# Performance work log

Measured on AMD Instinct MI355X. Metric: run time of the kernel, lower is better.

Reference implementation:

```python
import jax, jax.numpy as jnp
import numpy as np

IN_DIM, OUT_DIM, NUM, K = 256, 128, 16, 3
BATCH = 2048
MONO = ((0, 1), (1, -1))  # (input dim index, direction)


def _make_grid():
    # linspace over grid_range, then extend k knots on each side with uniform step h
    lo, hi = -1.0, 1.0
    h = (hi - lo) / NUM
    pts = np.linspace(lo, hi, NUM + 1)
    ext = np.concatenate([lo + h * np.arange(-K, 0), pts, hi + h * np.arange(1, K + 1)])
    return jnp.asarray(np.tile(ext, (IN_DIM, 1)), dtype=jnp.float32)  # (in_dim, num+2k+1)


def _b_batch(x, grid, k):
    # de-Boor B-spline basis. x: (B, in), grid: (in, G). Returns (B, in, G-k-1).
    xg = x[:, :, None]
    g = grid[None, :, :]
    B = ((xg >= g[:, :, :-1]) & (xg < g[:, :, 1:])).astype(x.dtype)
    for p in range(1, k + 1):
        left = (xg - g[:, :, :-(p + 1)]) / (g[:, :, p:-1] - g[:, :, :-(p + 1)]) * B[:, :, :-1]
        right = (g[:, :, p + 1:] - xg) / (g[:, :, p + 1:] - g[:, :, 1:-p]) * B[:, :, 1:]
        B = left + right
    return B


def setup_inputs() -> dict:
    key = jax.random.key(0)
    k1, k2, k3, k4 = jax.random.split(key, 4)
    inv_sqrt_in = 1.0 / np.sqrt(IN_DIM)
    x = 0.4 * jax.random.normal(k1, (BATCH, IN_DIM), dtype=jnp.float32)
    coef = 0.1 * jax.random.normal(k2, (IN_DIM, OUT_DIM, NUM + K), dtype=jnp.float32)
    scale_sp_raw = jnp.ones((IN_DIM, OUT_DIM), dtype=jnp.float32) * inv_sqrt_in
    scale_base = (jax.random.uniform(k3, (IN_DIM, OUT_DIM), dtype=jnp.float32) * 2.0 - 1.0) * inv_sqrt_in
    grid = _make_grid()
    mask = jnp.ones((IN_DIM, OUT_DIM), dtype=jnp.float32)
    base_mask = jnp.ones((IN_DIM, OUT_DIM), dtype=jnp.float32)
    for dim, _ in MONO:
        base_mask = base_mask.at[dim, :].set(0.0)
    return {"x": x, "coef": coef, "scale_sp_raw": scale_sp_raw, "scale_base": scale_base,
            "grid": grid, "mask": mask, "base_mask": base_mask}


def reference(x, coef, scale_sp_raw, scale_base, grid, mask, base_mask):
    bs = x.shape[0]
    preacts = jnp.broadcast_to(x[:, None, :], (bs, OUT_DIM, IN_DIM))
    # monotonic reparameterization: softplus + cumsum over spline-coefficient axis
    for dim, direction in MONO:
        delta = jnp.cumsum(jax.nn.softplus(coef[dim]), axis=-1)  # (out, num+k)
        coef = coef.at[dim].set(direction * delta)
    # coef2curve: basis (B, in, num+k) contracted with coef (in, out, num+k)
    basis = _b_batch(x, grid, K)
    y = jnp.einsum('bid,iod->bio', basis, coef)  # (B, in, out)
    postspline = jnp.transpose(y, (0, 2, 1))
    scale_sp = jax.nn.softplus(scale_sp_raw)
    y = scale_sp[None, :, :] * y
    base = base_mask * scale_base[None, :, :] * jax.nn.silu(x)[:, :, None]
    y = y + base
    y = mask[None, :, :] * y
    postacts = jnp.transpose(y, (0, 2, 1))
    out = jnp.sum(y, axis=1)  # (B, out)
    return out, preacts, postacts, postspline
```

## Files before the change

### kernel.cpp

```cpp
#include <hip/hip_runtime.h>
#include <math.h>

#define IN_DIM   256
#define OUT_DIM  128
#define NCOEF    19
#define BATCH    2048
#define BT       4

__device__ __forceinline__ float softplus_f(float v) {
  return (v > 20.0f) ? v : log1pf(expf(v));
}

__global__ void kan_prep(const float* __restrict__ coef,
                         const float* __restrict__ ssp,
                         const float* __restrict__ sbase,
                         const float* __restrict__ mask,
                         const float* __restrict__ bmask,
                         float* __restrict__ coefT,
                         float* __restrict__ At,
                         float* __restrict__ Bt) {
  int g = blockIdx.x * 256 + threadIdx.x;
  int o = g >> 8;
  int i = g & 255;
  const float* src = coef + ((size_t)i * OUT_DIM + o) * NCOEF;
  float c[NCOEF];
#pragma unroll
  for (int d = 0; d < NCOEF; ++d) c[d] = src[d];
  if (i < 2) {
    float dir = (i == 0) ? 1.0f : -1.0f;
    float acc = 0.0f;
#pragma unroll
    for (int d = 0; d < NCOEF; ++d) { acc += softplus_f(c[d]); c[d] = dir * acc; }
  }
  float* dst = coefT + (size_t)g * NCOEF;
#pragma unroll
  for (int d = 0; d < NCOEF; ++d) dst[d] = c[d];
  int io = i * OUT_DIM + o;
  float m = mask[io];
  At[g] = m * softplus_f(ssp[io]);
  Bt[g] = m * bmask[io] * sbase[io];
}

__device__ __forceinline__ float wave_reduce(float v) {
  int t;
  t = __builtin_amdgcn_update_dpp(0, __float_as_int(v), 0x111, 0xf, 0xf, true); v += __int_as_float(t);
  t = __builtin_amdgcn_update_dpp(0, __float_as_int(v), 0x112, 0xf, 0xf, true); v += __int_as_float(t);
  t = __builtin_amdgcn_update_dpp(0, __float_as_int(v), 0x114, 0xf, 0xf, true); v += __int_as_float(t);
  t = __builtin_amdgcn_update_dpp(0, __float_as_int(v), 0x118, 0xf, 0xf, true); v += __int_as_float(t);
  t = __builtin_amdgcn_update_dpp(0, __float_as_int(v), 0x142, 0xa, 0xf, true); v += __int_as_float(t);
  t = __builtin_amdgcn_update_dpp(0, __float_as_int(v), 0x143, 0xc, 0xf, true); v += __int_as_float(t);
  return v;
}

__global__ __launch_bounds__(512) void kan_main(
    const float* __restrict__ x,
    const float* __restrict__ coefT,
    const float* __restrict__ At,
    const float* __restrict__ Bt,
    float* __restrict__ out,
    float* __restrict__ preacts,
    float* __restrict__ postacts,
    float* __restrict__ postspline) {
  __shared__ __align__(16) float s_coef[IN_DIM * NCOEF];
  __shared__ float s_out[BT][OUT_DIM][4];

  const int tid  = threadIdx.x;
  const int i    = tid & 255;
  const int bsub = tid >> 8;
  const int wq   = (tid >> 6) & 3;
  const int b0   = blockIdx.x * BT;

  float xv[2], sl[2], wv[2][4];
  int   wi[2][4];

#pragma unroll
  for (int bb = 0; bb < 2; ++bb) {
    int b = b0 + bsub * 2 + bb;
    float xx = x[(size_t)b * IN_DIM + i];
    xv[bb] = xx;
    sl[bb] = xx / (1.0f + expf(-xx));

    float tpos = (xx + 1.375f) * 8.0f;
    int j = (int)floorf(tpos);
    bool valid = (j >= 0) && (j <= 21);
    int jc = valid ? j : 3;

    float N[4] = {1.0f, 0.0f, 0.0f, 0.0f};
#pragma unroll
    for (int p = 1; p <= 3; ++p) {
      const float inv = (p == 1) ? 8.0f : ((p == 2) ? 4.0f : (8.0f / 3.0f));
      float Np[4] = {0.0f, 0.0f, 0.0f, 0.0f};
#pragma unroll
      for (int m = 0; m < 4; ++m) {
        if (m <= p) {
          float ga = -1.375f + 0.125f * (float)(jc + m - p);
          float v = 0.0f;
          if (m > 0) v += (xx - ga) * inv * N[m - 1];
          if (m < p) v += ((ga + 0.125f * (float)(p + 1)) - xx) * inv * N[m];
          Np[m] = v;
        }
      }
#pragma unroll
      for (int m = 0; m < 4; ++m) N[m] = Np[m];
    }
#pragma unroll
    for (int r = 0; r < 4; ++r) {
      int dr = jc - 3 + r;
      bool ok = valid && (dr >= 0) && (dr <= 18);
      wv[bb][r] = ok ? N[r] : 0.0f;
      wi[bb][r] = i * NCOEF + (ok ? dr : 0);
    }
  }

  for (int o = 0; o < OUT_DIM; ++o) {
    __syncthreads();
    {
      const float4* src4 = (const float4*)(coefT + (size_t)o * (IN_DIM * NCOEF));
      float4* dst4 = (float4*)s_coef;
      for (int t = tid; t < (IN_DIM * NCOEF) / 4; t += 512) dst4[t] = src4[t];
    }
    __syncthreads();

    float a_sc = At[o * IN_DIM + i];
    float b_sc = Bt[o * IN_DIM + i];

#pragma unroll
    for (int bb = 0; bb < 2; ++bb) {
      int bl = bsub * 2 + bb;
      float sp = wv[bb][0] * s_coef[wi[bb][0]]
               + wv[bb][1] * s_coef[wi[bb][1]]
               + wv[bb][2] * s_coef[wi[bb][2]]
               + wv[bb][3] * s_coef[wi[bb][3]];
      float ya = a_sc * sp + b_sc * sl[bb];

      size_t off = (((size_t)(b0 + bl) * OUT_DIM) + o) * IN_DIM + i;
      __builtin_nontemporal_store(sp,     postspline + off);
      __builtin_nontemporal_store(ya,     postacts   + off);
      __builtin_nontemporal_store(xv[bb], preacts    + off);

      float red = wave_reduce(ya);
      if ((tid & 63) == 63) s_out[bl][o][wq] = red;
    }
  }

  __syncthreads();
  {
    int bl = tid >> 7;
    int o  = tid & 127;
    float s = s_out[bl][o][0] + s_out[bl][o][1] + s_out[bl][o][2] + s_out[bl][o][3];
    out[(size_t)(b0 + bl) * OUT_DIM + o] = s;
  }
}

extern "C" void kernel_launch(void* const* d_in, const int* in_sizes, int n_in,
                              void* d_out, int out_size, void* d_ws, size_t ws_size,
                              hipStream_t stream) {
  (void)in_sizes; (void)n_in; (void)out_size; (void)ws_size;

  const float* x     = (const float*)d_in[0];
  const float* coef  = (const float*)d_in[1];
  const float* ssp   = (const float*)d_in[2];
  const float* sbase = (const float*)d_in[3];
  const float* mask  = (const float*)d_in[5];
  const float* bmask = (const float*)d_in[6];

  float* coefT = (float*)d_ws;
  float* At    = coefT + (size_t)OUT_DIM * IN_DIM * NCOEF;
  float* Bt    = At + (size_t)OUT_DIM * IN_DIM;

  float* out        = (float*)d_out;
  float* preacts    = out + (size_t)BATCH * OUT_DIM;
  float* postacts   = preacts + (size_t)BATCH * OUT_DIM * IN_DIM;
  float* postspline = postacts + (size_t)BATCH * OUT_DIM * IN_DIM;

  kan_prep<<<(OUT_DIM * IN_DIM) / 256, 256, 0, stream>>>(coef, ssp, sbase, mask, bmask,
                                                         coefT, At, Bt);
  kan_main<<<BATCH / BT, 512, 0, stream>>>(x, coefT, At, Bt,
                                           out, preacts, postacts, postspline);
}
```

Measured before the change: 209.5 us.

## Double-buffer coefficient tiles in LDS with async global_load_lds prefetch

Replaces the per-output-column synchronous copy of the coefficient tile into shared memory with a two-buffer scheme. The next tile is fetched directly into LDS with the gfx950 global_load_lds builtin while the current tile is being used, and the per-column scale loads for the next column are prefetched into registers. This removes one barrier per iteration and aims to hide coefficient-load latency behind the large nontemporal output stores. It doubles LDS usage, which may reduce occupancy, and relies on the barrier also waiting for the async LDS loads.

Result: faster. 178.4 us (-14.9%).

```diff
diff --git a/kernel.cpp b/kernel.cpp
--- a/kernel.cpp
+++ b/kernel.cpp
@@ -6,9 +6,17 @@
 #define NCOEF    19
 #define BATCH    2048
 #define BT       4
+#define TILE_F   (IN_DIM * NCOEF)
 
 __device__ __forceinline__ float softplus_f(float v) {
   return (v > 20.0f) ? v : log1pf(expf(v));
+}
+
+__device__ __forceinline__ void load_lds16(const float* g, float* l) {
+  __builtin_amdgcn_global_load_lds(
+      (const __attribute__((address_space(1))) void*)g,
+      (__attribute__((address_space(3))) void*)l,
+      16, 0, 0);
 }
 
 __global__ void kan_prep(const float* __restrict__ coef,
@@ -61,7 +69,7 @@
     float* __restrict__ preacts,
     float* __restrict__ postacts,
     float* __restrict__ postspline) {
-  __shared__ __align__(16) float s_coef[IN_DIM * NCOEF];
+  __shared__ __align__(16) float s_coef[2][TILE_F];
   __shared__ float s_out[BT][OUT_DIM][4];
 
   const int tid  = threadIdx.x;
@@ -112,28 +120,47 @@
     }
   }
 
+  {
+    const float* src = coefT;
+    float* dst = &s_coef[0][0];
+    load_lds16(src + tid * 4,        dst + tid * 4);
+    load_lds16(src + 2048 + tid * 4, dst + 2048 + tid * 4);
+    if (tid < 192) load_lds16(src + 4096 + tid * 4, dst + 4096 + tid * 4);
+  }
+  float a_cur = At[i];
+  float b_cur = Bt[i];
+  __syncthreads();
+
+  size_t off0 = ((size_t)(b0 + bsub * 2)     * OUT_DIM) * IN_DIM + i;
+  size_t off1 = ((size_t)(b0 + bsub * 2 + 1) * OUT_DIM) * IN_DIM + i;
+
   for (int o = 0; o < OUT_DIM; ++o) {
-    __syncthreads();
-    {
-      const float4* src4 = (const float4*)(coefT + (size_t)o * (IN_DIM * NCOEF));
-      float4* dst4 = (float4*)s_coef;
-      for (int t = tid; t < (IN_DIM * NCOEF) / 4; t += 512) dst4[t] = src4[t];
-    }
-    __syncthreads();
-
-    float a_sc = At[o * IN_DIM + i];
-    float b_sc = Bt[o * IN_DIM + i];
+    const int cur = o & 1;
+    const float* sc = &s_coef[cur][0];
+
+    if (o + 1 < OUT_DIM) {
+      const float* src = coefT + (size_t)(o + 1) * TILE_F;
+      float* dst = &s_coef[cur ^ 1][0];
+      load_lds16(src + tid * 4,        dst + tid * 4);
+      load_lds16(src + 2048 + tid * 4, dst + 2048 + tid * 4);
+      if (tid < 192) load_lds16(src + 4096 + tid * 4, dst + 4096 + tid * 4);
+    }
+    float a_nxt = 0.0f, b_nxt = 0.0f;
+    if (o + 1 < OUT_DIM) {
+      a_nxt = At[(o + 1) * IN_DIM + i];
+      b_nxt = Bt[(o + 1) * IN_DIM + i];
+    }
 
 #pragma unroll
     for (int bb = 0; bb < 2; ++bb) {
       int bl = bsub * 2 + bb;
-      float sp = wv[bb][0] * s_coef[wi[bb][0]]
-               + wv[bb][1] * s_coef[wi[bb][1]]
-               + wv[bb][2] * s_coef[wi[bb][2]]
-               + wv[bb][3] * s_coef[wi[bb][3]];
-      float ya = a_sc * sp + b_sc * sl[bb];
-
-      size_t off = (((size_t)(b0 + bl) * OUT_DIM) + o) * IN_DIM + i;
+      float sp = wv[bb][0] * sc[wi[bb][0]]
+               + wv[bb][1] * sc[wi[bb][1]]
+               + wv[bb][2] * sc[wi[bb][2]]
+               + wv[bb][3] * sc[wi[bb][3]];
+      float ya = a_cur * sp + b_cur * sl[bb];
+
+      size_t off = (bb == 0 ? off0 : off1) + (size_t)o * IN_DIM;
       __builtin_nontemporal_store(sp,     postspline + off);
       __builtin_nontemporal_store(ya,     postacts   + off);
       __builtin_nontemporal_store(xv[bb], preacts    + off);
@@ -141,9 +168,12 @@
       float red = wave_reduce(ya);
       if ((tid & 63) == 63) s_out[bl][o][wq] = red;
     }
-  }
-
-  __syncthreads();
+
+    __syncthreads();
+    a_cur = a_nxt;
+    b_cur = b_nxt;
+  }
+
   {
     int bl = tid >> 7;
     int o  = tid & 127;
```

## Replace shared-memory coef staging with direct register gathers and prefetch

Applied to the files above, without the earlier changes.

Drops the per-output cooperative copy of the 19 KB coefficient tile into LDS and the two block barriers around it. Each thread now gathers its four needed coefficients per batch row straight from global memory (L2/L1 cached). Those loads are double-buffered one output ahead so they overlap the stores. It also sets a min-blocks occupancy hint, freeing the large LDS footprint to allow more resident blocks. The cost is scattered, uncoalesced global gathers in place of vectorized bulk copies.

Measured after the change: 298.2 us. 42.3% more time.

```diff
diff --git a/kernel.cpp b/kernel.cpp
--- a/kernel.cpp
+++ b/kernel.cpp
@@ -6,6 +6,7 @@
 #define NCOEF    19
 #define BATCH    2048
 #define BT       4
+#define TILE_F   (IN_DIM * NCOEF)
 
 __device__ __forceinline__ float softplus_f(float v) {
   return (v > 20.0f) ? v : log1pf(expf(v));
@@ -52,7 +53,7 @@
   return v;
 }
 
-__global__ __launch_bounds__(512) void kan_main(
+__global__ __launch_bounds__(512, 4) void kan_main(
     const float* __restrict__ x,
     const float* __restrict__ coefT,
     const float* __restrict__ At,
@@ -61,7 +62,6 @@
     float* __restrict__ preacts,
     float* __restrict__ postacts,
     float* __restrict__ postspline) {
-  __shared__ __align__(16) float s_coef[IN_DIM * NCOEF];
   __shared__ float s_out[BT][OUT_DIM][4];
 
   const int tid  = threadIdx.x;
@@ -112,36 +112,60 @@
     }
   }
 
-  for (int o = 0; o < OUT_DIM; ++o) {
-    __syncthreads();
+  size_t off0 = ((size_t)(b0 + bsub * 2)     * OUT_DIM) * IN_DIM + i;
+  size_t off1 = ((size_t)(b0 + bsub * 2 + 1) * OUT_DIM) * IN_DIM + i;
+
+  float cA[2][4], cB[2][4];
+  float aA, bA, aB, bB;
+#pragma unroll
+  for (int bb = 0; bb < 2; ++bb)
+#pragma unroll
+    for (int r = 0; r < 4; ++r) cA[bb][r] = coefT[wi[bb][r]];
+  aA = At[i];
+  bA = Bt[i];
+
+#define KAN_BODY(o_, C_, A_, B_)                                          \
+  do {                                                                    \
+    _Pragma("unroll")                                                     \
+    for (int bb = 0; bb < 2; ++bb) {                                      \
+      int bl = bsub * 2 + bb;                                             \
+      float sp = wv[bb][0] * C_[bb][0] + wv[bb][1] * C_[bb][1]            \
+               + wv[bb][2] * C_[bb][2] + wv[bb][3] * C_[bb][3];           \
+      float ya = A_ * sp + B_ * sl[bb];                                   \
+      size_t off = (bb == 0 ? off0 : off1) + (size_t)(o_) * IN_DIM;       \
+      __builtin_nontemporal_store(sp,     postspline + off);              \
+      __builtin_nontemporal_store(ya,     postacts   + off);              \
+      __builtin_nontemporal_store(xv[bb], preacts    + off);              \
+      float red = wave_reduce(ya);                                        \
+      if ((tid & 63) == 63) s_out[bl][o_][wq] = red;                      \
+    }                                                                     \
+  } while (0)
+
+  for (int oo = 0; oo < OUT_DIM; oo += 2) {
     {
-      const float4* src4 = (const float4*)(coefT + (size_t)o * (IN_DIM * NCOEF));
-      float4* dst4 = (float4*)s_coef;
-      for (int t = tid; t < (IN_DIM * NCOEF) / 4; t += 512) dst4[t] = src4[t];
-    }
-    __syncthreads();
-
-    float a_sc = At[o * IN_DIM + i];
-    float b_sc = Bt[o * IN_DIM + i];
-
-#pragma unroll
-    for (int bb = 0; bb < 2; ++bb) {
-      int bl = bsub * 2 + bb;
-      float sp = wv[bb][0] * s_coef[wi[bb][0]]
-               + wv[bb][1] * s_coef[wi[bb][1]]
-               + wv[bb][2] * s_coef[wi[bb][2]]
-               + wv[bb][3] * s_coef[wi[bb][3]];
-      float ya = a_sc * sp + b_sc * sl[bb];
-
-      size_t off = (((size_t)(b0 + bl) * OUT_DIM) + o) * IN_DIM + i;
-      __builtin_nontemporal_store(sp,     postspline + off);
-      __builtin_nontemporal_store(ya,     postacts   + off);
-      __builtin_nontemporal_store(xv[bb], preacts    + off);
-
-      float red = wave_reduce(ya);
-      if ((tid & 63) == 63) s_out[bl][o][wq] = red;
-    }
-  }
+      const int on = oo + 1;
+      const float* cpn = coefT + (size_t)on * TILE_F;
+#pragma unroll
+      for (int bb = 0; bb < 2; ++bb)
+#pragma unroll
+        for (int r = 0; r < 4; ++r) cB[bb][r] = cpn[wi[bb][r]];
+      aB = At[on * IN_DIM + i];
+      bB = Bt[on * IN_DIM + i];
+      KAN_BODY(oo, cA, aA, bA);
+    }
+    {
+      const int on = (oo + 2 < OUT_DIM) ? oo + 2 : OUT_DIM - 1;
+      const float* cpn = coefT + (size_t)on * TILE_F;
+#pragma unroll
+      for (int bb = 0; bb < 2; ++bb)
+#pragma unroll
+        for (int r = 0; r < 4; ++r) cA[bb][r] = cpn[wi[bb][r]];
+      aA = At[on * IN_DIM + i];
+      bA = Bt[on * IN_DIM + i];
+      KAN_BODY(oo + 1, cB, aB, bB);
+    }
+  }
+#undef KAN_BODY
 
   __syncthreads();
   {
```

## Double-buffer coefficient tiles via direct-to-LDS loads and vectorize per-thread outputs

Applied to the files above, without the earlier changes.

The coefficient table is re-laid out into padded 64x77 tiles per output, so each tile can be streamed straight into LDS with global_load_lds. The tiles are double-buffered, and one wait plus one barrier per output replaces the two full barriers per iteration. Each thread now handles four input dims of one batch row, so all three big outputs are written as 16-byte nontemporal vector stores. Each wave writes its row-sum straight to out, which removes the shared-memory reduction. The risks are the hand-tuned vmcnt accounting and the smaller 256-thread blocks.

Measured after the change: 207.0 us. Within noise of the previous version (-1.2%).

```diff
diff --git a/kernel.cpp b/kernel.cpp
--- a/kernel.cpp
+++ b/kernel.cpp
@@ -6,9 +6,28 @@
 #define NCOEF    19
 #define BATCH    2048
 #define BT       4
+#define QSTRIDE  77
+#define TILE_F   (64 * QSTRIDE)
+
+typedef float f32x4 __attribute__((ext_vector_type(4)));
 
 __device__ __forceinline__ float softplus_f(float v) {
   return (v > 20.0f) ? v : log1pf(expf(v));
+}
+
+__device__ __forceinline__ void load_lds16(const float* g, float* l) {
+  __builtin_amdgcn_global_load_lds(
+      (const __attribute__((address_space(1))) void*)g,
+      (__attribute__((address_space(3))) void*)l,
+      16, 0, 0);
+}
+
+__device__ __forceinline__ void stage_tile(const float* src, float* dst, int tid) {
+  load_lds16(src + tid * 4,        dst + tid * 4);
+  load_lds16(src + 1024 + tid * 4, dst + 1024 + tid * 4);
+  load_lds16(src + 2048 + tid * 4, dst + 2048 + tid * 4);
+  load_lds16(src + 3072 + tid * 4, dst + 3072 + tid * 4);
+  load_lds16(src + 3904 + tid * 4, dst + 3904 + tid * 4);
 }
 
 __global__ void kan_prep(const float* __restrict__ coef,
@@ -32,9 +51,10 @@
 #pragma unroll
     for (int d = 0; d < NCOEF; ++d) { acc += softplus_f(c[d]); c[d] = dir * acc; }
   }
-  float* dst = coefT + (size_t)g * NCOEF;
+  float* dst = coefT + (size_t)o * TILE_F + (i >> 2) * QSTRIDE + (i & 3) * NCOEF;
 #pragma unroll
   for (int d = 0; d < NCOEF; ++d) dst[d] = c[d];
+  if ((i & 3) == 3) dst[NCOEF] = 0.0f;
   int io = i * OUT_DIM + o;
   float m = mask[io];
   At[g] = m * softplus_f(ssp[io]);
@@ -52,7 +72,7 @@
   return v;
 }
 
-__global__ __launch_bounds__(512) void kan_main(
+__global__ __launch_bounds__(256, 2) void kan_main(
     const float* __restrict__ x,
     const float* __restrict__ coefT,
     const float* __restrict__ At,
@@ -61,24 +81,23 @@
     float* __restrict__ preacts,
     float* __restrict__ postacts,
     float* __restrict__ postspline) {
-  __shared__ __align__(16) float s_coef[IN_DIM * NCOEF];
-  __shared__ float s_out[BT][OUT_DIM][4];
+  __shared__ __align__(16) float s_coef[2][TILE_F];
 
   const int tid  = threadIdx.x;
-  const int i    = tid & 255;
-  const int bsub = tid >> 8;
-  const int wq   = (tid >> 6) & 3;
-  const int b0   = blockIdx.x * BT;
-
-  float xv[2], sl[2], wv[2][4];
-  int   wi[2][4];
-
-#pragma unroll
-  for (int bb = 0; bb < 2; ++bb) {
-    int b = b0 + bsub * 2 + bb;
-    float xx = x[(size_t)b * IN_DIM + i];
-    xv[bb] = xx;
-    sl[bb] = xx / (1.0f + expf(-xx));
+  const int lane = tid & 63;
+  const int w    = tid >> 6;
+  const int b    = blockIdx.x * BT + w;
+  const int i0   = lane * 4;
+
+  const f32x4 xv4 = *(const f32x4*)(x + (size_t)b * IN_DIM + i0);
+  float xv[4] = {xv4.x, xv4.y, xv4.z, xv4.w};
+  float sl[4], wv[4][4];
+  int   wl[4][4];
+
+#pragma unroll
+  for (int rr = 0; rr < 4; ++rr) {
+    float xx = xv[rr];
+    sl[rr] = xx / (1.0f + expf(-xx));
 
     float tpos = (xx + 1.375f) * 8.0f;
     int j = (int)floorf(tpos);
@@ -107,48 +126,57 @@
     for (int r = 0; r < 4; ++r) {
       int dr = jc - 3 + r;
       bool ok = valid && (dr >= 0) && (dr <= 18);
-      wv[bb][r] = ok ? N[r] : 0.0f;
-      wi[bb][r] = i * NCOEF + (ok ? dr : 0);
+      wv[rr][r] = ok ? N[r] : 0.0f;
+      wl[rr][r] = lane * QSTRIDE + rr * NCOEF + (ok ? dr : 0);
     }
   }
 
+  stage_tile(coefT, &s_coef[0][0], tid);
+  f32x4 a4 = *(const f32x4*)(At + i0);
+  f32x4 b4 = *(const f32x4*)(Bt + i0);
+  __syncthreads();
+
+  const size_t obase = ((size_t)b * OUT_DIM) * IN_DIM + i0;
+
+#pragma unroll 2
   for (int o = 0; o < OUT_DIM; ++o) {
-    __syncthreads();
-    {
-      const float4* src4 = (const float4*)(coefT + (size_t)o * (IN_DIM * NCOEF));
-      float4* dst4 = (float4*)s_coef;
-      for (int t = tid; t < (IN_DIM * NCOEF) / 4; t += 512) dst4[t] = src4[t];
-    }
-    __syncthreads();
-
-    float a_sc = At[o * IN_DIM + i];
-    float b_sc = Bt[o * IN_DIM + i];
-
-#pragma unroll
-    for (int bb = 0; bb < 2; ++bb) {
-      int bl = bsub * 2 + bb;
-      float sp = wv[bb][0] * s_coef[wi[bb][0]]
-               + wv[bb][1] * s_coef[wi[bb][1]]
-               + wv[bb][2] * s_coef[wi[bb][2]]
-               + wv[bb][3] * s_coef[wi[bb][3]];
-      float ya = a_sc * sp + b_sc * sl[bb];
-
-      size_t off = (((size_t)(b0 + bl) * OUT_DIM) + o) * IN_DIM + i;
-      __builtin_nontemporal_store(sp,     postspline + off);
-      __builtin_nontemporal_store(ya,     postacts   + off);
-      __builtin_nontemporal_store(xv[bb], preacts    + off);
-
-      float red = wave_reduce(ya);
-      if ((tid & 63) == 63) s_out[bl][o][wq] = red;
-    }
-  }
-
-  __syncthreads();
-  {
-    int bl = tid >> 7;
-    int o  = tid & 127;
-    float s = s_out[bl][o][0] + s_out[bl][o][1] + s_out[bl][o][2] + s_out[bl][o][3];
-    out[(size_t)(b0 + bl) * OUT_DIM + o] = s;
+    const float* sc = &s_coef[o & 1][0];
+
+    if (o + 1 < OUT_DIM)
+      stage_tile(coefT + (size_t)(o + 1) * TILE_F, &s_coef[(o & 1) ^ 1][0], tid);
+    asm volatile("" ::: "memory");
+
+    f32x4 a4n = a4, b4n = b4;
+    if (o + 1 < OUT_DIM) {
+      a4n = *(const f32x4*)(At + (o + 1) * IN_DIM + i0);
+      b4n = *(const f32x4*)(Bt + (o + 1) * IN_DIM + i0);
+    }
+
+    float sp[4], ya[4];
+#pragma unroll
+    for (int rr = 0; rr < 4; ++rr) {
+      sp[rr] = wv[rr][0] * sc[wl[rr][0]] + wv[rr][1] * sc[wl[rr][1]]
+             + wv[rr][2] * sc[wl[rr][2]] + wv[rr][3] * sc[wl[rr][3]];
+    }
+    ya[0] = a4.x * sp[0] + b4.x * sl[0];
+    ya[1] = a4.y * sp[1] + b4.y * sl[1];
+    ya[2] = a4.z * sp[2] + b4.z * sl[2];
+    ya[3] = a4.w * sp[3] + b4.w * sl[3];
+
+    size_t off = obase + (size_t)o * IN_DIM;
+    f32x4 sp4 = {sp[0], sp[1], sp[2], sp[3]};
+    f32x4 ya4 = {ya[0], ya[1], ya[2], ya[3]};
+    __builtin_nontemporal_store(sp4, (f32x4*)(postspline + off));
+    __builtin_nontemporal_store(ya4, (f32x4*)(postacts + off));
+    __builtin_nontemporal_store(xv4, (f32x4*)(preacts + off));
+
+    float red = wave_reduce((ya[0] + ya[1]) + (ya[2] + ya[3]));
+    if (lane == 63) out[(size_t)b * OUT_DIM + o] = red;
+
+    asm volatile("s_waitcnt vmcnt(4)" ::: "memory");
+    __builtin_amdgcn_s_barrier();
+
+    a4 = a4n; b4 = b4n;
   }
 }
 
@@ -165,7 +193,7 @@
   const float* bmask = (const float*)d_in[6];
 
   float* coefT = (float*)d_ws;
-  float* At    = coefT + (size_t)OUT_DIM * IN_DIM * NCOEF;
+  float* At    = coefT + (size_t)OUT_DIM * TILE_F;
   float* Bt    = At + (size_t)OUT_DIM * IN_DIM;
 
   float* out        = (float*)d_out;
@@ -175,6 +203,6 @@
 
   kan_prep<<<(OUT_DIM * IN_DIM) / 256, 256, 0, stream>>>(coef, ssp, sbase, mask, bmask,
                                                          coefT, At, Bt);
-  kan_main<<<BATCH / BT, 512, 0, stream>>>(x, coefT, At, Bt,
+  kan_main<<<BATCH / BT, 256, 0, stream>>>(x, coefT, At, Bt,
                                            out, preacts, postacts, postspline);
 }
```
